# Optimization experiments

Hardware: AMD Instinct MI355X
Metric: run time of the kernel (lower is better)

Reference implementation:

```python
import jax, jax.numpy as jnp
import numpy as np

NODE = 100000
REL = 2000
E = 600000  # n_edges == triple_size
D = 128
DEPTH = 2
HEADS = 1


def setup_inputs() -> dict:
    key = jax.random.key(0)
    ks = jax.random.split(key, 8)
    features = jax.random.normal(ks[0], (NODE, D), jnp.float32)
    rel_emb = jax.random.normal(ks[1], (REL, D), jnp.float32)
    sp_val = jax.random.uniform(ks[2], (E,), jnp.float32)
    attn_kernels = jax.random.normal(ks[3], (DEPTH, HEADS, 3 * D), jnp.float32) * 0.1
    adj_src = jnp.sort(jax.random.randint(ks[4], (E,), 0, NODE))  # tf.segment_sum needs sorted ids
    adj_dst = jax.random.randint(ks[5], (E,), 0, NODE)
    sp_rel = jax.random.randint(ks[6], (E,), 0, REL)
    sp_row = jnp.arange(E)  # sparse (triple, rel) matrix row indices
    return dict(features=features, rel_emb=rel_emb, sp_val=sp_val,
                attn_kernels=attn_kernels, adj_src=adj_src, adj_dst=adj_dst,
                sp_rel=sp_rel, sp_row=sp_row)


def _segment_softmax(logits, seg, num):
    m = jax.ops.segment_max(logits, seg, num_segments=num)
    e = jnp.exp(logits - m[seg])
    s = jax.ops.segment_sum(e, seg, num_segments=num)
    return e / s[seg]


def reference(features, rel_emb, sp_val, attn_kernels, adj_src, adj_dst, sp_rel, sp_row):
    act = jax.nn.relu
    feats = act(features)
    outputs = [feats]
    for l in range(DEPTH):
        heads = []
        for h in range(HEADS):
            ak = attn_kernels[l, h]  # [3D]
            # sparse (triple x rel) @ rel_emb -> per-edge relation embedding [E, D]
            rels = jax.ops.segment_sum(sp_val[:, None] * rel_emb[sp_rel], sp_row,
                                       num_segments=E)
            # tf.nn.l2_normalize with eps 1e-12
            rels = rels * jax.lax.rsqrt(jnp.maximum(jnp.sum(rels * rels, axis=1,
                                                            keepdims=True), 1e-12))
            neighs = feats[adj_dst]  # [E, D]
            selfs = feats[adj_src]   # [E, D]
            # Householder-style reflection of neighbor features across rels
            proj = jnp.sum(neighs * rels, axis=1, keepdims=True) * rels
            neighs = neighs - 2.0 * proj
            # attention logits: concat([selfs, neighs, rels]) @ ak
            att = selfs @ ak[:D] + neighs @ ak[D:2 * D] + rels @ ak[2 * D:]
            a = _segment_softmax(att, adj_src, NODE)  # tf.sparse_softmax per row
            heads.append(jax.ops.segment_sum(neighs * a[:, None], adj_src,
                                             num_segments=NODE))
        feats = heads[0] if HEADS == 1 else jnp.concatenate(heads, axis=1)
        feats = act(feats)
        outputs.append(feats)
    return jnp.concatenate(outputs, axis=1)  # [NODE, D*(DEPTH+1)]
```

## Files before the change

### kernel.cpp

```cpp
#include <hip/hip_runtime.h>
#include <math.h>
#include <stdint.h>

#define NNODE 100000
#define NREL 2000
#define NEDGE 600000
#define DIM 128
#define OUTC 384
#define LOG2E 1.4426950408889634f

#define RELU_BLOCKS 12500
#define PRE_BLOCKS 500
#define ROW_BLOCKS ((NNODE + 1 + 255) / 256)

typedef float f32x2 __attribute__((ext_vector_type(2)));

__device__ __forceinline__ float wave_sum(float v) {
#pragma unroll
    for (int off = 32; off > 0; off >>= 1)
        v += __shfl_xor(v, off, 64);
    return v;
}

__device__ __forceinline__ unsigned short f2bf(float f) {
    unsigned b = __float_as_uint(f);
    return (unsigned short)((b + 0x7fffu + ((b >> 16) & 1u)) >> 16);
}
__device__ __forceinline__ unsigned pack2(float f0, float f1) {
    return (unsigned)f2bf(f0) | ((unsigned)f2bf(f1) << 16);
}
__device__ __forceinline__ f32x2 bf2(unsigned u) {
    f32x2 r;
    r.x = __uint_as_float(u << 16);
    r.y = __uint_as_float(u & 0xffff0000u);
    return r;
}

__global__ void k_setup(const float* __restrict__ f, const float* __restrict__ rel,
                        const float* __restrict__ attn, const int* __restrict__ adj_src,
                        float* __restrict__ out, unsigned short* __restrict__ fm,
                        unsigned short* __restrict__ relm,
                        float* __restrict__ relnorm2, float* __restrict__ rdB,
                        float* __restrict__ rdC,
                        float* __restrict__ nd0, int* __restrict__ row_ptr) {
    int b = blockIdx.x;
    if (b < RELU_BLOCKS) {
        int idx = b * 256 + threadIdx.x;
        int n = idx >> 5;
        int q = idx & 31;
        float4 v = reinterpret_cast<const float4*>(f + (size_t)n * DIM)[q];
        v.x = fmaxf(v.x, 0.f); v.y = fmaxf(v.y, 0.f);
        v.z = fmaxf(v.z, 0.f); v.w = fmaxf(v.w, 0.f);
        reinterpret_cast<float4*>(out + (size_t)n * OUTC)[q] = v;
        uint2 p;
        p.x = pack2(v.x, v.y);
        p.y = pack2(v.z, v.w);
        reinterpret_cast<uint2*>(fm + (size_t)n * DIM)[q] = p;
        float4 bb = reinterpret_cast<const float4*>(attn + DIM)[q];
        float pb = v.x * bb.x + v.y * bb.y + v.z * bb.z + v.w * bb.w;
#pragma unroll
        for (int off = 1; off <= 16; off <<= 1)
            pb += __shfl_xor(pb, off, 64);
        if (q == 0) nd0[n] = pb * LOG2E;
    } else if (b < RELU_BLOCKS + PRE_BLOCKS) {
        int wid = (b - RELU_BLOCKS) * 4 + (threadIdx.x >> 6);
        int lane = threadIdx.x & 63;
        float2 v = reinterpret_cast<const float2*>(rel + (size_t)wid * DIM)[lane];
        reinterpret_cast<unsigned*>(relm + (size_t)wid * DIM)[lane] = pack2(v.x, v.y);
        float2 b0 = reinterpret_cast<const float2*>(attn + DIM)[lane];
        float2 c0 = reinterpret_cast<const float2*>(attn + 2 * DIM)[lane];
        float2 b1 = reinterpret_cast<const float2*>(attn + 3 * DIM + DIM)[lane];
        float2 c1 = reinterpret_cast<const float2*>(attn + 3 * DIM + 2 * DIM)[lane];
        float n2  = wave_sum(v.x * v.x + v.y * v.y);
        float pb0 = wave_sum(v.x * b0.x + v.y * b0.y);
        float pc0 = wave_sum(v.x * c0.x + v.y * c0.y);
        float pb1 = wave_sum(v.x * b1.x + v.y * b1.y);
        float pc1 = wave_sum(v.x * c1.x + v.y * c1.y);
        if (lane == 0) {
            relnorm2[wid] = n2;
            rdB[wid] = pb0;        rdC[wid] = pc0;
            rdB[NREL + wid] = pb1; rdC[NREL + wid] = pc1;
        }
    } else {
        int n = (b - RELU_BLOCKS - PRE_BLOCKS) * 256 + threadIdx.x;
        if (n <= NNODE) {
            int lo = 0, hi = NEDGE;
            while (lo < hi) {
                int mid = (lo + hi) >> 1;
                if (adj_src[mid] < n) lo = mid + 1; else hi = mid;
            }
            row_ptr[n] = lo;
        }
    }
}

__global__ void k_edges(const float* __restrict__ sp_val, const int* __restrict__ sp_rel,
                        const int* __restrict__ adj_dst,
                        const float* __restrict__ relnorm2,
                        const float* __restrict__ rdB, const float* __restrict__ rdC,
                        const float* __restrict__ nd0,
                        float4* __restrict__ ed0, float4* __restrict__ ed1) {
    int e = blockIdx.x * blockDim.x + threadIdx.x;
    if (e >= NEDGE) return;
    float v = sp_val[e];
    int r = sp_rel[e];
    int dst = adj_dst[e];
    float n2 = relnorm2[r];
    float sc = v * rsqrtf(fmaxf(v * v * n2, 1e-12f));
    float q2 = 2.f * sc * sc;
    float scl = sc * LOG2E, q2l = q2 * LOG2E;
    unsigned pk = ((unsigned)dst << 11) | (unsigned)r;
    float pkf = __uint_as_float(pk);
    ed0[e] = make_float4(nd0[dst] + scl * rdC[r], q2l * rdB[r], q2, pkf);
    ed1[e] = make_float4(scl * rdC[NREL + r], q2l * rdB[NREL + r], q2, pkf);
}

template<int USE_ED, int NDFOLD, int WRITE_NEXT>
__global__ void k_gat(const unsigned short* __restrict__ fin_m,
                      float* __restrict__ fout,
                      unsigned short* __restrict__ fout_m,
                      const unsigned short* __restrict__ relm,
                      const float4* __restrict__ edata,
                      const int* __restrict__ adj_dst, const int* __restrict__ sp_rel,
                      const float* __restrict__ sp_val, const float* __restrict__ relnorm2,
                      const float* __restrict__ rdB, const float* __restrict__ rdC,
                      const float* __restrict__ ndpre,
                      const int* __restrict__ row_ptr,
                      float* __restrict__ nd_n,
                      const float* __restrict__ akB_next) {
    int wv = (blockIdx.x * blockDim.x + threadIdx.x) >> 6;
    int lane = threadIdx.x & 63;
    int g = lane >> 4, gl = lane & 15;
    int node = wv * 4 + g;
    if (node >= NNODE) return;
    int e0 = row_ptr[node], e1 = row_ptr[node + 1];

    f32x2 acc0 = 0.f, acc1 = 0.f, acc2 = 0.f, acc3 = 0.f;
    float s = 0.f;

    uint4 fb = make_uint4(0, 0, 0, 0), rb = make_uint4(0, 0, 0, 0);
    float ab = 0.f, qb = 0.f, q2 = 0.f;
    int e = e0;
    if (e < e1) {
        int dst, r;
        if (USE_ED) {
            float4 ed = edata[e];
            unsigned pk = __float_as_uint(ed.w);
            dst = (int)(pk >> 11); r = (int)(pk & 2047u);
            ab = NDFOLD ? ed.x : ed.x + ndpre[dst];
            qb = ed.y; q2 = ed.z;
        } else {
            dst = adj_dst[e]; r = sp_rel[e];
            float v = sp_val[e];
            float sc = v * rsqrtf(fmaxf(v * v * relnorm2[r], 1e-12f));
            q2 = 2.f * sc * sc;
            qb = q2 * LOG2E * rdB[r];
            ab = ndpre[dst] + sc * LOG2E * rdC[r];
        }
        fb = *reinterpret_cast<const uint4*>(fin_m + (unsigned)((dst << 7) + (gl << 3)));
        rb = *reinterpret_cast<const uint4*>(relm + (unsigned)((r << 7) + (gl << 3)));
    }
    while (e < e1) {
        int en = e + 1;
        uint4 fb2 = make_uint4(0, 0, 0, 0), rb2 = make_uint4(0, 0, 0, 0);
        float ab2 = 0.f, qb2 = 0.f, q22 = 0.f;
        if (en < e1) {
            int dst, r;
            if (USE_ED) {
                float4 ed = edata[en];
                unsigned pk = __float_as_uint(ed.w);
                dst = (int)(pk >> 11); r = (int)(pk & 2047u);
                ab2 = NDFOLD ? ed.x : ed.x + ndpre[dst];
                qb2 = ed.y; q22 = ed.z;
            } else {
                dst = adj_dst[en]; r = sp_rel[en];
                float v = sp_val[en];
                float sc = v * rsqrtf(fmaxf(v * v * relnorm2[r], 1e-12f));
                q22 = 2.f * sc * sc;
                qb2 = q22 * LOG2E * rdB[r];
                ab2 = ndpre[dst] + sc * LOG2E * rdC[r];
            }
            fb2 = *reinterpret_cast<const uint4*>(fin_m + (unsigned)((dst << 7) + (gl << 3)));
            rb2 = *reinterpret_cast<const uint4*>(relm + (unsigned)((r << 7) + (gl << 3)));
        }
        f32x2 f0 = bf2(fb.x), f1 = bf2(fb.y), f2 = bf2(fb.z), f3 = bf2(fb.w);
        f32x2 r0 = bf2(rb.x), r1 = bf2(rb.y), r2 = bf2(rb.z), r3 = bf2(rb.w);
        f32x2 d2 = f0 * r0;
        d2 += f1 * r1;
        d2 += f2 * r2;
        d2 += f3 * r3;
        float dot = d2.x + d2.y;
        dot += __shfl_xor(dot, 1, 64);
        dot += __shfl_xor(dot, 2, 64);
        dot += __shfl_xor(dot, 4, 64);
        dot += __shfl_xor(dot, 8, 64);
        float w = __builtin_exp2f(ab - dot * qb);
        float k2 = dot * q2;
        s += w;
        acc0 += w * (f0 - k2 * r0);
        acc1 += w * (f1 - k2 * r1);
        acc2 += w * (f2 - k2 * r2);
        acc3 += w * (f3 - k2 * r3);
        e = en;
        fb = fb2; rb = rb2; ab = ab2; qb = qb2; q2 = q22;
    }

    float inv = (s > 0.f) ? 1.f / s : 0.f;
    float o[8];
    o[0] = fmaxf(acc0.x * inv, 0.f); o[1] = fmaxf(acc0.y * inv, 0.f);
    o[2] = fmaxf(acc1.x * inv, 0.f); o[3] = fmaxf(acc1.y * inv, 0.f);
    o[4] = fmaxf(acc2.x * inv, 0.f); o[5] = fmaxf(acc2.y * inv, 0.f);
    o[6] = fmaxf(acc3.x * inv, 0.f); o[7] = fmaxf(acc3.y * inv, 0.f);
    float4* op = reinterpret_cast<float4*>(fout + (unsigned)(node * OUTC + gl * 8));
    op[0] = make_float4(o[0], o[1], o[2], o[3]);
    op[1] = make_float4(o[4], o[5], o[6], o[7]);
    if (WRITE_NEXT) {
        uint4 mw;
        mw.x = pack2(o[0], o[1]); mw.y = pack2(o[2], o[3]);
        mw.z = pack2(o[4], o[5]); mw.w = pack2(o[6], o[7]);
        *reinterpret_cast<uint4*>(fout_m + (unsigned)((node << 7) + (gl << 3))) = mw;
        const float4* aB = reinterpret_cast<const float4*>(akB_next) + gl * 2;
        float4 b0 = aB[0], b1 = aB[1];
        float pb = o[0] * b0.x + o[1] * b0.y + o[2] * b0.z + o[3] * b0.w
                 + o[4] * b1.x + o[5] * b1.y + o[6] * b1.z + o[7] * b1.w;
#pragma unroll
        for (int off = 1; off <= 8; off <<= 1)
            pb += __shfl_xor(pb, off, 64);
        if (gl == 0) nd_n[node] = pb * LOG2E;
    }
}

extern "C" void kernel_launch(void* const* d_in, const int* in_sizes, int n_in,
                              void* d_out, int out_size, void* d_ws, size_t ws_size,
                              hipStream_t stream) {
    const float* features = (const float*)d_in[0];
    const float* rel_emb  = (const float*)d_in[1];
    const float* sp_val   = (const float*)d_in[2];
    const float* attn     = (const float*)d_in[3];
    const int*   adj_src  = (const int*)d_in[4];
    const int*   adj_dst  = (const int*)d_in[5];
    const int*   sp_rel   = (const int*)d_in[6];
    float* out = (float*)d_out;

    char* p = (char*)d_ws;
    unsigned short* mir0 = (unsigned short*)p; p += (size_t)NNODE * DIM * 2;
    unsigned short* mir1 = (unsigned short*)p; p += (size_t)NNODE * DIM * 2;
    unsigned short* relm = (unsigned short*)p; p += (size_t)NREL * DIM * 2;
    float* nd0      = (float*)p; p += (size_t)NNODE * 4;
    float* nd1      = (float*)p; p += (size_t)NNODE * 4;
    float* relnorm2 = (float*)p; p += (size_t)NREL * 4;
    float* rdB      = (float*)p; p += (size_t)2 * NREL * 4;
    float* rdC      = (float*)p; p += (size_t)2 * NREL * 4;
    int*   row_ptr  = (int*)p;   p += (size_t)(NNODE + 1) * 4;
    p = (char*)(((uintptr_t)p + 15) & ~(uintptr_t)15);
    float4* ed0 = (float4*)p; p += (size_t)NEDGE * 16;
    float4* ed1 = (float4*)p; p += (size_t)NEDGE * 16;
    size_t needed = (size_t)(p - (char*)d_ws);
    bool use_ed = (ws_size >= needed);

    k_setup<<<RELU_BLOCKS + PRE_BLOCKS + ROW_BLOCKS, 256, 0, stream>>>(
        features, rel_emb, attn, adj_src, out, mir0, relm,
        relnorm2, rdB, rdC, nd0, row_ptr);

    int gat_blocks = (NNODE / 4 * 64) / 256;
    const float* akB1 = attn + 3 * DIM + DIM;

    if (use_ed) {
        k_edges<<<(NEDGE + 255) / 256, 256, 0, stream>>>(
            sp_val, sp_rel, adj_dst, relnorm2, rdB, rdC, nd0, ed0, ed1);
        k_gat<1, 1, 1><<<gat_blocks, 256, 0, stream>>>(
            mir0, out + DIM, mir1, relm, ed0, adj_dst, sp_rel, sp_val, relnorm2,
            rdB, rdC, nd0, row_ptr, nd1, akB1);
        k_gat<1, 0, 0><<<gat_blocks, 256, 0, stream>>>(
            mir1, out + 2 * DIM, (unsigned short*)nullptr, relm, ed1, adj_dst, sp_rel,
            sp_val, relnorm2, rdB + NREL, rdC + NREL, nd1, row_ptr,
            (float*)nullptr, (const float*)nullptr);
    } else {
        k_gat<0, 0, 1><<<gat_blocks, 256, 0, stream>>>(
            mir0, out + DIM, mir1, relm, (const float4*)nullptr, adj_dst, sp_rel,
            sp_val, relnorm2, rdB, rdC, nd0, row_ptr, nd1, akB1);
        k_gat<0, 0, 0><<<gat_blocks, 256, 0, stream>>>(
            mir1, out + 2 * DIM, (unsigned short*)nullptr, relm, (const float4*)nullptr,
            adj_dst, sp_rel, sp_val, relnorm2, rdB + NREL, rdC + NREL, nd1, row_ptr,
            (float*)nullptr, (const float*)nullptr);
    }
}
```

Baseline: 144.8 us.

## Deepen edge prefetch, use DPP reductions, fold layer-2 node term in pass

```diff
diff --git a/kernel.cpp b/kernel.cpp
--- a/kernel.cpp
+++ b/kernel.cpp
@@ -20,6 +20,14 @@
     for (int off = 32; off > 0; off >>= 1)
         v += __shfl_xor(v, off, 64);
     return v;
+}
+
+__device__ __forceinline__ float dpp_sum16(float x) {
+    x += __int_as_float(__builtin_amdgcn_mov_dpp(__float_as_int(x), 0xB1, 0xF, 0xF, true));
+    x += __int_as_float(__builtin_amdgcn_mov_dpp(__float_as_int(x), 0x4E, 0xF, 0xF, true));
+    x += __int_as_float(__builtin_amdgcn_mov_dpp(__float_as_int(x), 0x124, 0xF, 0xF, true));
+    x += __int_as_float(__builtin_amdgcn_mov_dpp(__float_as_int(x), 0x128, 0xF, 0xF, true));
+    return x;
 }
 
 __device__ __forceinline__ unsigned short f2bf(float f) {
@@ -115,19 +123,28 @@
     ed1[e] = make_float4(scl * rdC[NREL + r], q2l * rdB[NREL + r], q2, pkf);
 }
 
-template<int USE_ED, int NDFOLD, int WRITE_NEXT>
-__global__ void k_gat(const unsigned short* __restrict__ fin_m,
-                      float* __restrict__ fout,
-                      unsigned short* __restrict__ fout_m,
-                      const unsigned short* __restrict__ relm,
-                      const float4* __restrict__ edata,
-                      const int* __restrict__ adj_dst, const int* __restrict__ sp_rel,
-                      const float* __restrict__ sp_val, const float* __restrict__ relnorm2,
-                      const float* __restrict__ rdB, const float* __restrict__ rdC,
-                      const float* __restrict__ ndpre,
-                      const int* __restrict__ row_ptr,
-                      float* __restrict__ nd_n,
-                      const float* __restrict__ akB_next) {
+__global__ void k_fold(float4* __restrict__ ed, const float* __restrict__ nd) {
+    int e = blockIdx.x * blockDim.x + threadIdx.x;
+    if (e >= NEDGE) return;
+    float4 v = ed[e];
+    unsigned pk = __float_as_uint(v.w);
+    ed[e].x = v.x + nd[pk >> 11];
+}
+
+template<int USE_ED, int WRITE_NEXT>
+__global__ __launch_bounds__(256, 8)
+void k_gat(const unsigned short* __restrict__ fin_m,
+           float* __restrict__ fout,
+           unsigned short* __restrict__ fout_m,
+           const unsigned short* __restrict__ relm,
+           const float4* __restrict__ edata,
+           const int* __restrict__ adj_dst, const int* __restrict__ sp_rel,
+           const float* __restrict__ sp_val, const float* __restrict__ relnorm2,
+           const float* __restrict__ rdB, const float* __restrict__ rdC,
+           const float* __restrict__ ndpre,
+           const int* __restrict__ row_ptr,
+           float* __restrict__ nd_n,
+           const float* __restrict__ akB_next) {
     int wv = (blockIdx.x * blockDim.x + threadIdx.x) >> 6;
     int lane = threadIdx.x & 63;
     int g = lane >> 4, gl = lane & 15;
@@ -138,71 +155,57 @@
     f32x2 acc0 = 0.f, acc1 = 0.f, acc2 = 0.f, acc3 = 0.f;
     float s = 0.f;
 
-    uint4 fb = make_uint4(0, 0, 0, 0), rb = make_uint4(0, 0, 0, 0);
-    float ab = 0.f, qb = 0.f, q2 = 0.f;
-    int e = e0;
-    if (e < e1) {
-        int dst, r;
-        if (USE_ED) {
-            float4 ed = edata[e];
-            unsigned pk = __float_as_uint(ed.w);
-            dst = (int)(pk >> 11); r = (int)(pk & 2047u);
-            ab = NDFOLD ? ed.x : ed.x + ndpre[dst];
-            qb = ed.y; q2 = ed.z;
-        } else {
-            dst = adj_dst[e]; r = sp_rel[e];
-            float v = sp_val[e];
-            float sc = v * rsqrtf(fmaxf(v * v * relnorm2[r], 1e-12f));
-            q2 = 2.f * sc * sc;
-            qb = q2 * LOG2E * rdB[r];
-            ab = ndpre[dst] + sc * LOG2E * rdC[r];
-        }
-        fb = *reinterpret_cast<const uint4*>(fin_m + (unsigned)((dst << 7) + (gl << 3)));
-        rb = *reinterpret_cast<const uint4*>(relm + (unsigned)((r << 7) + (gl << 3)));
-    }
-    while (e < e1) {
-        int en = e + 1;
-        uint4 fb2 = make_uint4(0, 0, 0, 0), rb2 = make_uint4(0, 0, 0, 0);
-        float ab2 = 0.f, qb2 = 0.f, q22 = 0.f;
-        if (en < e1) {
+    auto ld = [&](int ee, uint4& fb_, uint4& rb_, float& ab_, float& qb_, float& q2_) {
+        fb_ = make_uint4(0, 0, 0, 0); rb_ = make_uint4(0, 0, 0, 0);
+        ab_ = 0.f; qb_ = 0.f; q2_ = 0.f;
+        if (ee < e1) {
             int dst, r;
             if (USE_ED) {
-                float4 ed = edata[en];
+                float4 ed = edata[ee];
                 unsigned pk = __float_as_uint(ed.w);
                 dst = (int)(pk >> 11); r = (int)(pk & 2047u);
-                ab2 = NDFOLD ? ed.x : ed.x + ndpre[dst];
-                qb2 = ed.y; q22 = ed.z;
+                ab_ = ed.x; qb_ = ed.y; q2_ = ed.z;
             } else {
-                dst = adj_dst[en]; r = sp_rel[en];
-                float v = sp_val[en];
+                dst = adj_dst[ee]; r = sp_rel[ee];
+                float v = sp_val[ee];
                 float sc = v * rsqrtf(fmaxf(v * v * relnorm2[r], 1e-12f));
-                q22 = 2.f * sc * sc;
-                qb2 = q22 * LOG2E * rdB[r];
-                ab2 = ndpre[dst] + sc * LOG2E * rdC[r];
+                q2_ = 2.f * sc * sc;
+                qb_ = q2_ * LOG2E * rdB[r];
+                ab_ = ndpre[dst] + sc * LOG2E * rdC[r];
             }
-            fb2 = *reinterpret_cast<const uint4*>(fin_m + (unsigned)((dst << 7) + (gl << 3)));
-            rb2 = *reinterpret_cast<const uint4*>(relm + (unsigned)((r << 7) + (gl << 3)));
+            fb_ = *reinterpret_cast<const uint4*>(fin_m + (unsigned)((dst << 7) + (gl << 3)));
+            rb_ = *reinterpret_cast<const uint4*>(relm + (unsigned)((r << 7) + (gl << 3)));
         }
-        f32x2 f0 = bf2(fb.x), f1 = bf2(fb.y), f2 = bf2(fb.z), f3 = bf2(fb.w);
-        f32x2 r0 = bf2(rb.x), r1 = bf2(rb.y), r2 = bf2(rb.z), r3 = bf2(rb.w);
+    };
+
+    uint4 fbA, rbA, fbB, rbB;
+    float abA, qbA, q2A, abB, qbB, q2B;
+    int e = e0;
+    ld(e, fbA, rbA, abA, qbA, q2A);
+    ld(e + 1, fbB, rbB, abB, qbB, q2B);
+    while (e < e1) {
+        uint4 fbC, rbC;
+        float abC, qbC, q2C;
+        ld(e + 2, fbC, rbC, abC, qbC, q2C);
+
+        f32x2 f0 = bf2(fbA.x), f1 = bf2(fbA.y), f2 = bf2(fbA.z), f3 = bf2(fbA.w);
+        f32x2 r0 = bf2(rbA.x), r1 = bf2(rbA.y), r2 = bf2(rbA.z), r3 = bf2(rbA.w);
         f32x2 d2 = f0 * r0;
         d2 += f1 * r1;
         d2 += f2 * r2;
         d2 += f3 * r3;
-        float dot = d2.x + d2.y;
-        dot += __shfl_xor(dot, 1, 64);
-        dot += __shfl_xor(dot, 2, 64);
-        dot += __shfl_xor(dot, 4, 64);
-        dot += __shfl_xor(dot, 8, 64);
-        float w = __builtin_exp2f(ab - dot * qb);
-        float k2 = dot * q2;
+        float dot = dpp_sum16(d2.x + d2.y);
+        float w = __builtin_exp2f(abA - dot * qbA);
+        float k2 = dot * q2A;
         s += w;
         acc0 += w * (f0 - k2 * r0);
         acc1 += w * (f1 - k2 * r1);
         acc2 += w * (f2 - k2 * r2);
         acc3 += w * (f3 - k2 * r3);
-        e = en;
-        fb = fb2; rb = rb2; ab = ab2; qb = qb2; q2 = q22;
+
+        fbA = fbB; rbA = rbB; abA = abB; qbA = qbB; q2A = q2B;
+        fbB = fbC; rbB = rbC; abB = abC; qbB = qbC; q2B = q2C;
+        ++e;
     }
 
     float inv = (s > 0.f) ? 1.f / s : 0.f;
@@ -223,9 +226,7 @@
         float4 b0 = aB[0], b1 = aB[1];
         float pb = o[0] * b0.x + o[1] * b0.y + o[2] * b0.z + o[3] * b0.w
                  + o[4] * b1.x + o[5] * b1.y + o[6] * b1.z + o[7] * b1.w;
-#pragma unroll
-        for (int off = 1; off <= 8; off <<= 1)
-            pb += __shfl_xor(pb, off, 64);
+        pb = dpp_sum16(pb);
         if (gl == 0) nd_n[node] = pb * LOG2E;
     }
 }
@@ -268,18 +269,19 @@
     if (use_ed) {
         k_edges<<<(NEDGE + 255) / 256, 256, 0, stream>>>(
             sp_val, sp_rel, adj_dst, relnorm2, rdB, rdC, nd0, ed0, ed1);
-        k_gat<1, 1, 1><<<gat_blocks, 256, 0, stream>>>(
+        k_gat<1, 1><<<gat_blocks, 256, 0, stream>>>(
             mir0, out + DIM, mir1, relm, ed0, adj_dst, sp_rel, sp_val, relnorm2,
             rdB, rdC, nd0, row_ptr, nd1, akB1);
-        k_gat<1, 0, 0><<<gat_blocks, 256, 0, stream>>>(
+        k_fold<<<(NEDGE + 255) / 256, 256, 0, stream>>>(ed1, nd1);
+        k_gat<1, 0><<<gat_blocks, 256, 0, stream>>>(
             mir1, out + 2 * DIM, (unsigned short*)nullptr, relm, ed1, adj_dst, sp_rel,
             sp_val, relnorm2, rdB + NREL, rdC + NREL, nd1, row_ptr,
             (float*)nullptr, (const float*)nullptr);
     } else {
-        k_gat<0, 0, 1><<<gat_blocks, 256, 0, stream>>>(
+        k_gat<0, 1><<<gat_blocks, 256, 0, stream>>>(
             mir0, out + DIM, mir1, relm, (const float4*)nullptr, adj_dst, sp_rel,
             sp_val, relnorm2, rdB, rdC, nd0, row_ptr, nd1, akB1);
-        k_gat<0, 0, 0><<<gat_blocks, 256, 0, stream>>>(
+        k_gat<0, 0><<<gat_blocks, 256, 0, stream>>>(
             mir1, out + 2 * DIM, (unsigned short*)nullptr, relm, (const float4*)nullptr,
             adj_dst, sp_rel, sp_val, relnorm2, rdB + NREL, rdC + NREL, nd1, row_ptr,
             (float*)nullptr, (const float*)nullptr);
```

New measurement: 140.2 us. 3.2% less time.
